# Kernel optimization log

Hardware: AMD Instinct MI355X
Metric: run time of the kernel (lower is better)

## Reference

```python
import jax, jax.numpy as jnp
import numpy as np

EMBED_SIZE = 1024
HEADS = 16
HEAD_DIM = EMBED_SIZE // HEADS


def setup_inputs() -> dict:
    key = jax.random.key(0)
    ks = jax.random.split(key, 9)
    N, L = 2, 2048
    inv = 1.0 / np.sqrt(HEAD_DIM)
    return {
        "values": jax.random.normal(ks[0], (N, L, EMBED_SIZE), dtype=jnp.float32),
        "keys": jax.random.normal(ks[1], (N, L, EMBED_SIZE), dtype=jnp.float32),
        "query": jax.random.normal(ks[2], (N, L, EMBED_SIZE), dtype=jnp.float32),
        "mask": jnp.ones((N, 1, 1, L), dtype=jnp.int32),
        # per-head projections: a single head_dim x head_dim weight shared across heads
        "Wv": jax.random.normal(ks[3], (HEAD_DIM, HEAD_DIM), dtype=jnp.float32) * inv,
        "Wk": jax.random.normal(ks[4], (HEAD_DIM, HEAD_DIM), dtype=jnp.float32) * inv,
        "Wq": jax.random.normal(ks[5], (HEAD_DIM, HEAD_DIM), dtype=jnp.float32) * inv,
        "Wo": jax.random.normal(ks[6], (EMBED_SIZE, EMBED_SIZE), dtype=jnp.float32) / np.sqrt(EMBED_SIZE),
        "bo": jnp.zeros((EMBED_SIZE,), dtype=jnp.float32),
    }


def reference(values, keys, query, mask, Wv, Wk, Wq, Wo, bo):
    N, q_len, E = query.shape
    k_len = keys.shape[1]
    v_len = values.shape[1]
    H, D = HEADS, HEAD_DIM

    v = values.reshape(N, v_len, H, D)
    k = keys.reshape(N, k_len, H, D)
    q = query.reshape(N, q_len, H, D)

    # nn.Linear(head_dim, head_dim, bias=False): y = x @ W.T, same W for every head
    v = jnp.einsum("nlhd,ed->nlhe", v, Wv)
    k = jnp.einsum("nlhd,ed->nlhe", k, Wk)
    q = jnp.einsum("nqhd,ed->nqhe", q, Wq)

    # full [N, H, Q, K] score matrix, as in the original
    energy = jnp.einsum("nqhd,nkhd->nhqk", q, k)
    energy = jnp.where(mask == 0, jnp.float32(-1e20), energy)

    # NOTE: scale is sqrt(embed_size), not sqrt(head_dim), applied after masking
    attention = jax.nn.softmax(energy / jnp.sqrt(jnp.float32(E)), axis=3)

    out = jnp.einsum("nhql,nlhd->nqhd", attention, v).reshape(N, q_len, H * D)
    out = out @ Wo.T + bo
    return out
```

## Files before the change

kernel.cpp:

```cpp
#include <hip/hip_runtime.h>

#define HEADS 16
#define HDIM 64
#define EMB 1024
#define SEQ 2048
#define NBATCH 2

typedef short short8 __attribute__((ext_vector_type(8)));
typedef float f32x4 __attribute__((ext_vector_type(4)));
typedef float f32x16 __attribute__((ext_vector_type(16)));

__device__ __forceinline__ unsigned short f2bf(float f) {
  unsigned u = __builtin_bit_cast(unsigned, f);
  u += 0x7fffu + ((u >> 16) & 1u);
  return (unsigned short)(u >> 16);
}

__device__ __forceinline__ unsigned cvtpk(float lo, float hi) {
  unsigned r;
  asm("v_cvt_pk_bf16_f32 %0, %1, %2" : "=v"(r) : "v"(lo), "v"(hi));
  return r;
}

__device__ __forceinline__ void swap32(unsigned& a, unsigned& b) {
  asm("v_permlane32_swap_b32 %0, %1" : "+v"(a), "+v"(b));
}

__global__ __launch_bounds__(256) void prep_kernel(
    const float* __restrict__ src, unsigned short* __restrict__ dst,
    const int* __restrict__ mask, float* __restrict__ biasf,
    int* __restrict__ flags, const float* __restrict__ Wq,
    const float* __restrict__ Wk, const float* __restrict__ Wv,
    unsigned short* __restrict__ wqkv, float qscale) {
  int b = blockIdx.x;
  int t = threadIdx.x;
  if (b < 1024) {
    int i = (b * 256 + t) * 4;
    float4 v = *(const float4*)(src + i);
    uint2 pk;
    pk.x = (unsigned)f2bf(v.x) | ((unsigned)f2bf(v.y) << 16);
    pk.y = (unsigned)f2bf(v.z) | ((unsigned)f2bf(v.w) << 16);
    *(uint2*)(dst + i) = pk;
  } else if (b < 1028) {
    int i = (b - 1024) * 1024 + t * 4;
    int4 m = *(const int4*)(mask + i);
    float4 o;
    o.x = m.x ? 0.0f : -1e30f;
    o.y = m.y ? 0.0f : -1e30f;
    o.z = m.z ? 0.0f : -1e30f;
    o.w = m.w ? 0.0f : -1e30f;
    *(float4*)(biasf + i) = o;
  } else if (b == 1028) {
    if (t < 64) {
      int n = t >> 5, tile = t & 31;
      const int* mp = mask + n * SEQ + tile * 64;
      int anyz = 0;
#pragma unroll
      for (int i = 0; i < 16; ++i) {
        int4 m = *(const int4*)(mp + i * 4);
        anyz |= (!m.x) | (!m.y) | (!m.z) | (!m.w);
      }
      flags[t] = anyz;
    }
  } else {
    int j = (b - 1029) * 1024 + t * 4;
    const float* s;
    int off = j;
    float sc = 1.0f;
    if (j < 4096) { s = Wq; sc = qscale; }
    else if (j < 8192) { s = Wk; off = j - 4096; }
    else { s = Wv; off = j - 8192; }
    float4 v = *(const float4*)(s + off);
    uint2 pk;
    pk.x = (unsigned)f2bf(v.x * sc) | ((unsigned)f2bf(v.y * sc) << 16);
    pk.y = (unsigned)f2bf(v.z * sc) | ((unsigned)f2bf(v.w * sc) << 16);
    *(uint2*)(wqkv + j) = pk;
  }
}

__global__ __launch_bounds__(256) void proj_kernel(
    const float* __restrict__ q_in, const float* __restrict__ k_in,
    const float* __restrict__ v_in, const unsigned short* __restrict__ wqkv,
    unsigned short* __restrict__ qp, unsigned short* __restrict__ kp,
    unsigned short* __restrict__ vt) {
  int t = threadIdx.x;
  int w = t >> 6, lane = t & 63;
  int l5 = lane & 31, hi = lane >> 5;

  __shared__ uint4 Wl[1536];
#pragma unroll
  for (int i = 0; i < 6; ++i) {
    int idx = i * 256 + t;
    int row = idx >> 3, c8 = idx & 7;
    Wl[row * 8 + (c8 ^ (row & 7))] = *(const uint4*)(wqkv + idx * 8);
  }
  __syncthreads();

  int d = (int)blockIdx.x;
  int work = (d & 7) * 192 + (d >> 3);
  int u = work * 4 + w;
  int rest = u / 3;
  int tensor = u - rest * 3;
  int l32 = rest & 63, h = (rest >> 6) & 15, n = rest >> 10;
  int lbase = l32 * 32;

  const float* x = tensor == 0 ? q_in : (tensor == 1 ? k_in : v_in);
  const float* xr = x + ((size_t)(n * SEQ + lbase + l5) * HEADS + h) * HDIM + hi * 8;

  short8 xf[4];
#pragma unroll
  for (int ds = 0; ds < 4; ++ds) {
    float4 a = *(const float4*)(xr + ds * 16);
    float4 bb = *(const float4*)(xr + ds * 16 + 4);
    uint4 u4;
    u4.x = cvtpk(a.x, a.y);
    u4.y = cvtpk(a.z, a.w);
    u4.z = cvtpk(bb.x, bb.y);
    u4.w = cvtpk(bb.z, bb.w);
    xf[ds] = __builtin_bit_cast(short8, u4);
  }

  const int rsw = l5 & 7;
  int wrow0 = tensor * 64 + l5;
  int wrow1 = wrow0 + 32;
  f32x16 acc0 = {}, acc1 = {};

  if (tensor < 2) {
#pragma unroll
    for (int ds = 0; ds < 4; ++ds) {
      short8 w0 = __builtin_bit_cast(short8, Wl[wrow0 * 8 + ((ds * 2 + hi) ^ rsw)]);
      short8 w1 = __builtin_bit_cast(short8, Wl[wrow1 * 8 + ((ds * 2 + hi) ^ rsw)]);
      acc0 = __builtin_amdgcn_mfma_f32_32x32x16_bf16(w0, xf[ds], acc0, 0, 0, 0);
      acc1 = __builtin_amdgcn_mfma_f32_32x32x16_bf16(w1, xf[ds], acc1, 0, 0, 0);
    }
    unsigned short* orow = (tensor == 0 ? qp : kp) +
        ((size_t)(n * HEADS + h) * SEQ + lbase + l5) * HDIM + hi * 4;
#pragma unroll
    for (int g = 0; g < 4; ++g) {
      uint2 o0, o1;
      o0.x = cvtpk(acc0[g * 4 + 0], acc0[g * 4 + 1]);
      o0.y = cvtpk(acc0[g * 4 + 2], acc0[g * 4 + 3]);
      o1.x = cvtpk(acc1[g * 4 + 0], acc1[g * 4 + 1]);
      o1.y = cvtpk(acc1[g * 4 + 2], acc1[g * 4 + 3]);
      *(uint2*)(orow + g * 8) = o0;
      *(uint2*)(orow + 32 + g * 8) = o1;
    }
  } else {
#pragma unroll
    for (int ds = 0; ds < 4; ++ds) {
      short8 w0 = __builtin_bit_cast(short8, Wl[wrow0 * 8 + ((ds * 2 + hi) ^ rsw)]);
      short8 w1 = __builtin_bit_cast(short8, Wl[wrow1 * 8 + ((ds * 2 + hi) ^ rsw)]);
      acc0 = __builtin_amdgcn_mfma_f32_32x32x16_bf16(xf[ds], w0, acc0, 0, 0, 0);
      acc1 = __builtin_amdgcn_mfma_f32_32x32x16_bf16(xf[ds], w1, acc1, 0, 0, 0);
    }
    unsigned short* vb = vt + (size_t)(n * HEADS + h) * HDIM * SEQ;
    unsigned short* r0 = vb + (size_t)l5 * SEQ + lbase + hi * 4;
    unsigned short* r1 = vb + (size_t)(32 + l5) * SEQ + lbase + hi * 4;
#pragma unroll
    for (int g = 0; g < 4; ++g) {
      uint2 o0, o1;
      o0.x = cvtpk(acc0[g * 4 + 0], acc0[g * 4 + 1]);
      o0.y = cvtpk(acc0[g * 4 + 2], acc0[g * 4 + 3]);
      o1.x = cvtpk(acc1[g * 4 + 0], acc1[g * 4 + 1]);
      o1.y = cvtpk(acc1[g * 4 + 2], acc1[g * 4 + 3]);
      *(uint2*)(r0 + g * 8) = o0;
      *(uint2*)(r1 + g * 8) = o1;
    }
  }
}

__global__ __launch_bounds__(512, 4) void attn_kernel(
    const unsigned short* __restrict__ qp, const unsigned short* __restrict__ kp,
    const unsigned short* __restrict__ vt, const float* __restrict__ biasf,
    const int* __restrict__ flags, unsigned short* __restrict__ ao) {
  int t = threadIdx.x;
  int w = t >> 6;
  int lane = t & 63;
  int l5 = lane & 31, hi = lane >> 5;
  int ks = w >> 2;
  int wq = w & 3;

  int d = (int)blockIdx.x;
  int work = (d & 7) * 64 + (d >> 3);
  int qs = work & 15;
  int h = (work >> 4) & 15;
  int n = work >> 8;
  int qw = qs * 128 + wq * 32;

  size_t slab = (size_t)(n * HEADS + h);
  const unsigned short* Qb = qp + slab * SEQ * HDIM;
  const unsigned short* Kb = kp + slab * SEQ * HDIM;
  const unsigned short* Vb = vt + slab * (size_t)HDIM * SEQ;
  const float* biasp = biasf + n * SEQ;
  const int* flagp = flags + n * 32;

  __shared__ uint4 Kl[2][2][512];
  __shared__ uint4 Vl[2][2][512];

  int tt = t & 255;

  auto STAGE = [&](int buf, int kb) {
#pragma unroll
    for (int i = 0; i < 2; ++i) {
      int idx = i * 256 + tt;
      int row = idx >> 3;
      int c8 = (idx & 7) ^ (row & 7);
      const unsigned short* gk = Kb + (size_t)(kb + row) * HDIM + c8 * 8;
      const unsigned short* gv = Vb + (size_t)row * SEQ + kb + c8 * 8;
      __builtin_amdgcn_global_load_lds(
          (const __attribute__((address_space(1))) unsigned*)gk,
          (__attribute__((address_space(3))) unsigned*)&Kl[ks][buf][i * 256 + (tt >> 6) * 64],
          16, 0, 0);
      __builtin_amdgcn_global_load_lds(
          (const __attribute__((address_space(1))) unsigned*)gv,
          (__attribute__((address_space(3))) unsigned*)&Vl[ks][buf][i * 256 + (tt >> 6) * 64],
          16, 0, 0);
    }
  };

  short8 bq[4];
  {
    const unsigned short* qrow = Qb + (size_t)(qw + l5) * HDIM + hi * 8;
#pragma unroll
    for (int dstep = 0; dstep < 4; ++dstep)
      bq[dstep] = __builtin_bit_cast(short8, *(const uint4*)(qrow + dstep * 16));
  }

  f32x16 acc0 = {}, acc1 = {};
  float lrun = 0.0f;
  const int rsw = l5 & 7;
  const float FM = 8.0f;
  int k0 = ks * (SEQ / 2);

  STAGE(0, k0);
  int cur = 0;

#pragma unroll 1
  for (int t8 = 0; t8 < SEQ / 2 / 64; ++t8) {
    int kb = k0 + t8 * 64;
    __syncthreads();
    if (t8 + 1 < SEQ / 2 / 64) STAGE(cur ^ 1, kb + 64);

    f32x16 s0 = {}, s1 = {};
    __builtin_amdgcn_s_setprio(1);
#pragma unroll
    for (int dstep = 0; dstep < 4; ++dstep) {
      short8 kf0 = __builtin_bit_cast(short8, Kl[ks][cur][l5 * 8 + ((dstep * 2 + hi) ^ rsw)]);
      short8 kf1 = __builtin_bit_cast(short8, Kl[ks][cur][256 + l5 * 8 + ((dstep * 2 + hi) ^ rsw)]);
      s0 = __builtin_amdgcn_mfma_f32_32x32x16_bf16(kf0, bq[dstep], s0, 0, 0, 0);
      s1 = __builtin_amdgcn_mfma_f32_32x32x16_bf16(kf1, bq[dstep], s1, 0, 0, 0);
    }
    __builtin_amdgcn_s_setprio(0);

    if (flagp[kb >> 6]) {
#pragma unroll
      for (int g = 0; g < 4; ++g) {
        f32x4 b0 = *(const f32x4*)(biasp + kb + g * 8 + hi * 4);
        f32x4 b1 = *(const f32x4*)(biasp + kb + 32 + g * 8 + hi * 4);
#pragma unroll
        for (int i = 0; i < 4; ++i) {
          s0[g * 4 + i] += b0[i];
          s1[g * 4 + i] += b1[i];
        }
      }
    }

    float ps = 0.0f;
    unsigned wv[16];
#pragma unroll
    for (int i = 0; i < 8; ++i) {
      float p0 = exp2f(s0[2 * i] - FM);
      float p1 = exp2f(s0[2 * i + 1] - FM);
      ps += p0 + p1;
      wv[i] = cvtpk(p0, p1);
    }
#pragma unroll
    for (int i = 0; i < 8; ++i) {
      float p0 = exp2f(s1[2 * i] - FM);
      float p1 = exp2f(s1[2 * i + 1] - FM);
      ps += p0 + p1;
      wv[8 + i] = cvtpk(p0, p1);
    }
    lrun += ps;

    short8 pf[4];
#pragma unroll
    for (int kt = 0; kt < 2; ++kt) {
#pragma unroll
      for (int s = 0; s < 2; ++s) {
        unsigned a = wv[kt * 8 + s * 4 + 0], c = wv[kt * 8 + s * 4 + 2];
        unsigned b = wv[kt * 8 + s * 4 + 1], dd = wv[kt * 8 + s * 4 + 3];
        swap32(a, c);
        swap32(b, dd);
        uint4 u = {a, b, c, dd};
        pf[kt * 2 + s] = __builtin_bit_cast(short8, u);
      }
    }

    __builtin_amdgcn_s_setprio(1);
#pragma unroll
    for (int ks4 = 0; ks4 < 4; ++ks4) {
      short8 v0 = __builtin_bit_cast(short8, Vl[ks][cur][l5 * 8 + ((ks4 * 2 + hi) ^ rsw)]);
      short8 v1 = __builtin_bit_cast(short8, Vl[ks][cur][256 + l5 * 8 + ((ks4 * 2 + hi) ^ rsw)]);
      acc0 = __builtin_amdgcn_mfma_f32_32x32x16_bf16(v0, pf[ks4], acc0, 0, 0, 0);
      acc1 = __builtin_amdgcn_mfma_f32_32x32x16_bf16(v1, pf[ks4], acc1, 0, 0, 0);
    }
    __builtin_amdgcn_s_setprio(0);
    cur ^= 1;
  }

  __syncthreads();
  float* cb = (float*)&Kl[0][0][0];
  float* lb = (float*)&Vl[0][0][0];
  if (w >= 4) {
    float* dst = cb + (w - 4) * 2048;
#pragma unroll
    for (int r = 0; r < 16; ++r) {
      dst[r * 64 + lane] = acc0[r];
      dst[(r + 16) * 64 + lane] = acc1[r];
    }
    lb[(w - 4) * 64 + lane] = lrun;
  }
  __syncthreads();
  if (w < 4) {
    const float* src = cb + w * 2048;
#pragma unroll
    for (int r = 0; r < 16; ++r) {
      acc0[r] += src[r * 64 + lane];
      acc1[r] += src[(r + 16) * 64 + lane];
    }
    lrun += lb[w * 64 + lane];
    float lt = lrun + __shfl_xor(lrun, 32, 64);
    float inv = 1.0f / lt;

    unsigned short* obase =
        ao + ((size_t)(n * SEQ + qw + l5)) * EMB + h * HDIM + hi * 4;
#pragma unroll
    for (int g = 0; g < 4; ++g) {
      uint2 o0, o1;
      o0.x = cvtpk(acc0[g * 4 + 0] * inv, acc0[g * 4 + 1] * inv);
      o0.y = cvtpk(acc0[g * 4 + 2] * inv, acc0[g * 4 + 3] * inv);
      o1.x = cvtpk(acc1[g * 4 + 0] * inv, acc1[g * 4 + 1] * inv);
      o1.y = cvtpk(acc1[g * 4 + 2] * inv, acc1[g * 4 + 3] * inv);
      *(uint2*)(obase + g * 8) = o0;
      *(uint2*)(obase + 32 + g * 8) = o1;
    }
  }
}

__global__ __launch_bounds__(256) void gemm_bt_kernel(
    const unsigned short* __restrict__ A, const unsigned short* __restrict__ B,
    const float* __restrict__ bias, float* __restrict__ Cm) {
  int t = threadIdx.x;
  int lane = t & 63, w = t >> 6;
  int lr = lane & 15, lg = lane >> 4;
  int m0 = blockIdx.y * 128, n0 = blockIdx.x * 64;
  int wr = w >> 1, wc = w & 1;

  __shared__ uint4 Al[1024];
  __shared__ uint4 Bl[512];

  f32x4 zero = {0.0f, 0.0f, 0.0f, 0.0f};
  f32x4 acc[4][2];
#pragma unroll
  for (int mt = 0; mt < 4; ++mt)
#pragma unroll
    for (int nt = 0; nt < 2; ++nt) acc[mt][nt] = zero;

  for (int kt = 0; kt < EMB; kt += 64) {
    __syncthreads();
#pragma unroll
    for (int s = 0; s < 4; ++s) {
      int c = t + s * 256;
      int row = c >> 3, c16 = c & 7;
      uint4 v = *(const uint4*)(A + (size_t)(m0 + row) * EMB + kt + c16 * 8);
      Al[(row * 8 + c16) ^ (row & 7)] = v;
    }
#pragma unroll
    for (int s = 0; s < 2; ++s) {
      int c = t + s * 256;
      int row = c >> 3, c16 = c & 7;
      uint4 v = *(const uint4*)(B + (size_t)(n0 + row) * EMB + kt + c16 * 8);
      Bl[(row * 8 + c16) ^ (row & 7)] = v;
    }
    __syncthreads();
#pragma unroll
    for (int kk = 0; kk < 2; ++kk) {
      short8 af[4], bfr[2];
#pragma unroll
      for (int mt = 0; mt < 4; ++mt) {
        int row = wr * 64 + mt * 16 + lr;
        af[mt] = __builtin_bit_cast(short8, Al[(row * 8 + kk * 4 + lg) ^ (row & 7)]);
      }
#pragma unroll
      for (int nt = 0; nt < 2; ++nt) {
        int row = wc * 32 + nt * 16 + lr;
        bfr[nt] = __builtin_bit_cast(short8, Bl[(row * 8 + kk * 4 + lg) ^ (row & 7)]);
      }
#pragma unroll
      for (int mt = 0; mt < 4; ++mt)
#pragma unroll
        for (int nt = 0; nt < 2; ++nt)
          acc[mt][nt] = __builtin_amdgcn_mfma_f32_16x16x32_bf16(af[mt], bfr[nt],
                                                                acc[mt][nt], 0, 0, 0);
    }
  }

#pragma unroll
  for (int nt = 0; nt < 2; ++nt) {
    int col = n0 + wc * 32 + nt * 16 + lr;
    float bv = bias[col];
#pragma unroll
    for (int mt = 0; mt < 4; ++mt) {
#pragma unroll
      for (int i = 0; i < 4; ++i) {
        int rowm = m0 + wr * 64 + mt * 16 + lg * 4 + i;
        Cm[(size_t)rowm * EMB + col] = acc[mt][nt][i] + bv;
      }
    }
  }
}

extern "C" void kernel_launch(void* const* d_in, const int* in_sizes, int n_in,
                              void* d_out, int out_size, void* d_ws, size_t ws_size,
                              hipStream_t stream) {
  const float* values = (const float*)d_in[0];
  const float* keys   = (const float*)d_in[1];
  const float* query  = (const float*)d_in[2];
  const int*   mask   = (const int*)d_in[3];
  const float* Wv     = (const float*)d_in[4];
  const float* Wk     = (const float*)d_in[5];
  const float* Wq     = (const float*)d_in[6];
  const float* Wo     = (const float*)d_in[7];
  const float* bo     = (const float*)d_in[8];
  float* out = (float*)d_out;

  const size_t slab = (size_t)NBATCH * HEADS * SEQ * HDIM;
  unsigned short* qp  = (unsigned short*)d_ws;
  unsigned short* kp  = qp + slab;
  unsigned short* vt  = kp + slab;
  unsigned short* ao  = vt + slab;
  unsigned short* wob = ao + slab;
  float* biasf = (float*)(wob + (size_t)EMB * EMB);
  int* flags = (int*)(biasf + NBATCH * SEQ);
  unsigned short* wqkv = (unsigned short*)(flags + 64);

  float qscale = 1.4426950408889634f / 32.0f;

  prep_kernel<<<dim3(1041), 256, 0, stream>>>(Wo, wob, mask, biasf, flags,
                                              Wq, Wk, Wv, wqkv, qscale);
  proj_kernel<<<dim3(1536), 256, 0, stream>>>(query, keys, values, wqkv, qp, kp, vt);
  attn_kernel<<<dim3((SEQ / 128) * HEADS * NBATCH), 512, 0, stream>>>(
      qp, kp, vt, biasf, flags, ao);
  gemm_bt_kernel<<<dim3(EMB / 64, (NBATCH * SEQ) / 128), 256, 0, stream>>>(ao, wob, bo, out);
}
```

Before: 108.4 us.

## Double-buffer output GEMM with direct global-to-LDS loads and unroll attention loop by two

```diff
diff --git a/kernel.cpp b/kernel.cpp
--- a/kernel.cpp
+++ b/kernel.cpp
@@ -232,21 +232,13 @@
   const float FM = 8.0f;
   int k0 = ks * (SEQ / 2);
 
-  STAGE(0, k0);
-  int cur = 0;
-
-#pragma unroll 1
-  for (int t8 = 0; t8 < SEQ / 2 / 64; ++t8) {
-    int kb = k0 + t8 * 64;
-    __syncthreads();
-    if (t8 + 1 < SEQ / 2 / 64) STAGE(cur ^ 1, kb + 64);
-
+  auto TILE = [&](int buf, int kb) __attribute__((always_inline)) {
     f32x16 s0 = {}, s1 = {};
     __builtin_amdgcn_s_setprio(1);
 #pragma unroll
     for (int dstep = 0; dstep < 4; ++dstep) {
-      short8 kf0 = __builtin_bit_cast(short8, Kl[ks][cur][l5 * 8 + ((dstep * 2 + hi) ^ rsw)]);
-      short8 kf1 = __builtin_bit_cast(short8, Kl[ks][cur][256 + l5 * 8 + ((dstep * 2 + hi) ^ rsw)]);
+      short8 kf0 = __builtin_bit_cast(short8, Kl[ks][buf][l5 * 8 + ((dstep * 2 + hi) ^ rsw)]);
+      short8 kf1 = __builtin_bit_cast(short8, Kl[ks][buf][256 + l5 * 8 + ((dstep * 2 + hi) ^ rsw)]);
       s0 = __builtin_amdgcn_mfma_f32_32x32x16_bf16(kf0, bq[dstep], s0, 0, 0, 0);
       s1 = __builtin_amdgcn_mfma_f32_32x32x16_bf16(kf1, bq[dstep], s1, 0, 0, 0);
     }
@@ -300,13 +292,25 @@
     __builtin_amdgcn_s_setprio(1);
 #pragma unroll
     for (int ks4 = 0; ks4 < 4; ++ks4) {
-      short8 v0 = __builtin_bit_cast(short8, Vl[ks][cur][l5 * 8 + ((ks4 * 2 + hi) ^ rsw)]);
-      short8 v1 = __builtin_bit_cast(short8, Vl[ks][cur][256 + l5 * 8 + ((ks4 * 2 + hi) ^ rsw)]);
+      short8 v0 = __builtin_bit_cast(short8, Vl[ks][buf][l5 * 8 + ((ks4 * 2 + hi) ^ rsw)]);
+      short8 v1 = __builtin_bit_cast(short8, Vl[ks][buf][256 + l5 * 8 + ((ks4 * 2 + hi) ^ rsw)]);
       acc0 = __builtin_amdgcn_mfma_f32_32x32x16_bf16(v0, pf[ks4], acc0, 0, 0, 0);
       acc1 = __builtin_amdgcn_mfma_f32_32x32x16_bf16(v1, pf[ks4], acc1, 0, 0, 0);
     }
     __builtin_amdgcn_s_setprio(0);
-    cur ^= 1;
+  };
+
+  const int NT = SEQ / 2 / 64;
+  STAGE(0, k0);
+#pragma unroll 1
+  for (int p = 0; p < NT; p += 2) {
+    int kb = k0 + p * 64;
+    __syncthreads();
+    STAGE(1, kb + 64);
+    TILE(0, kb);
+    __syncthreads();
+    if (p + 2 < NT) STAGE(0, kb + 128);
+    TILE(1, kb + 64);
   }
 
   __syncthreads();
@@ -349,16 +353,45 @@
 }
 
 __global__ __launch_bounds__(256) void gemm_bt_kernel(
-    const unsigned short* __restrict__ A, const unsigned short* __restrict__ B,
+    const unsigned short* __restrict__ Ag, const unsigned short* __restrict__ Bg,
     const float* __restrict__ bias, float* __restrict__ Cm) {
   int t = threadIdx.x;
   int lane = t & 63, w = t >> 6;
   int lr = lane & 15, lg = lane >> 4;
-  int m0 = blockIdx.y * 128, n0 = blockIdx.x * 64;
   int wr = w >> 1, wc = w & 1;
 
-  __shared__ uint4 Al[1024];
-  __shared__ uint4 Bl[512];
+  int d = (int)blockIdx.x;
+  int work = (d & 7) * 64 + (d >> 3);
+  int bx = work & 15, by = work >> 4;
+  int m0 = by * 128, n0 = bx * 64;
+
+  __shared__ uint4 Al[2][1024];
+  __shared__ uint4 Bl[2][512];
+
+  int wu = __builtin_amdgcn_readfirstlane(w);
+
+  auto STAGE_G = [&](int buf, int kt) {
+#pragma unroll
+    for (int i = 0; i < 4; ++i) {
+      int idx = i * 256 + t;
+      int row = idx >> 3, c8 = (idx & 7) ^ (row & 7);
+      __builtin_amdgcn_global_load_lds(
+          (const __attribute__((address_space(1))) unsigned*)(
+              Ag + (size_t)(m0 + row) * EMB + kt + c8 * 8),
+          (__attribute__((address_space(3))) unsigned*)&Al[buf][i * 256 + wu * 64],
+          16, 0, 0);
+    }
+#pragma unroll
+    for (int i = 0; i < 2; ++i) {
+      int idx = i * 256 + t;
+      int row = idx >> 3, c8 = (idx & 7) ^ (row & 7);
+      __builtin_amdgcn_global_load_lds(
+          (const __attribute__((address_space(1))) unsigned*)(
+              Bg + (size_t)(n0 + row) * EMB + kt + c8 * 8),
+          (__attribute__((address_space(3))) unsigned*)&Bl[buf][i * 256 + wu * 64],
+          16, 0, 0);
+    }
+  };
 
   f32x4 zero = {0.0f, 0.0f, 0.0f, 0.0f};
   f32x4 acc[4][2];
@@ -367,35 +400,19 @@
 #pragma unroll
     for (int nt = 0; nt < 2; ++nt) acc[mt][nt] = zero;
 
-  for (int kt = 0; kt < EMB; kt += 64) {
-    __syncthreads();
-#pragma unroll
-    for (int s = 0; s < 4; ++s) {
-      int c = t + s * 256;
-      int row = c >> 3, c16 = c & 7;
-      uint4 v = *(const uint4*)(A + (size_t)(m0 + row) * EMB + kt + c16 * 8);
-      Al[(row * 8 + c16) ^ (row & 7)] = v;
-    }
-#pragma unroll
-    for (int s = 0; s < 2; ++s) {
-      int c = t + s * 256;
-      int row = c >> 3, c16 = c & 7;
-      uint4 v = *(const uint4*)(B + (size_t)(n0 + row) * EMB + kt + c16 * 8);
-      Bl[(row * 8 + c16) ^ (row & 7)] = v;
-    }
-    __syncthreads();
+  auto COMP = [&](int buf) __attribute__((always_inline)) {
 #pragma unroll
     for (int kk = 0; kk < 2; ++kk) {
       short8 af[4], bfr[2];
 #pragma unroll
       for (int mt = 0; mt < 4; ++mt) {
         int row = wr * 64 + mt * 16 + lr;
-        af[mt] = __builtin_bit_cast(short8, Al[(row * 8 + kk * 4 + lg) ^ (row & 7)]);
+        af[mt] = __builtin_bit_cast(short8, Al[buf][(row * 8 + kk * 4 + lg) ^ (row & 7)]);
       }
 #pragma unroll
       for (int nt = 0; nt < 2; ++nt) {
         int row = wc * 32 + nt * 16 + lr;
-        bfr[nt] = __builtin_bit_cast(short8, Bl[(row * 8 + kk * 4 + lg) ^ (row & 7)]);
+        bfr[nt] = __builtin_bit_cast(short8, Bl[buf][(row * 8 + kk * 4 + lg) ^ (row & 7)]);
       }
 #pragma unroll
       for (int mt = 0; mt < 4; ++mt)
@@ -404,6 +421,17 @@
           acc[mt][nt] = __builtin_amdgcn_mfma_f32_16x16x32_bf16(af[mt], bfr[nt],
                                                                 acc[mt][nt], 0, 0, 0);
     }
+  };
+
+  STAGE_G(0, 0);
+#pragma unroll 1
+  for (int kt = 0; kt < EMB; kt += 128) {
+    __syncthreads();
+    STAGE_G(1, kt + 64);
+    COMP(0);
+    __syncthreads();
+    if (kt + 128 < EMB) STAGE_G(0, kt + 128);
+    COMP(1);
   }
 
 #pragma unroll
@@ -452,5 +480,5 @@
   proj_kernel<<<dim3(1536), 256, 0, stream>>>(query, keys, values, wqkv, qp, kp, vt);
   attn_kernel<<<dim3((SEQ / 128) * HEADS * NBATCH), 512, 0, stream>>>(
       qp, kp, vt, biasf, flags, ao);
-  gemm_bt_kernel<<<dim3(EMB / 64, (NBATCH * SEQ) / 128), 256, 0, stream>>>(ao, wob, bo, out);
-}
+  gemm_bt_kernel<<<dim3(512), 256, 0, stream>>>(ao, wob, bo, out);
+}
```

Result: slower. 142.2 us (+31.2%).
